# Kernel tuning notes

Hardware: AMD Instinct MI355X
Metric: run time of the kernel (lower is better)

## Reference

```python
import jax, jax.numpy as jnp
import numpy as np

B, N, C, S = 16, 1024, 16, 8
TYPE_DIM, TOK_DIM, D, O = 128, 128, 256, 256
NUM_TYPES, NUM_TOKENS, L = 200, 50000, 2
NEG = -1000000000000.0


def setup_inputs() -> dict:
    key = jax.random.key(0)
    ks = jax.random.split(key, 8)
    node_type = jax.random.randint(ks[0], (B, N), 0, NUM_TYPES)
    node_tokens = jax.random.randint(ks[1], (B, N, S), 0, NUM_TOKENS)
    children_index = jax.random.randint(ks[2], (B, N, C), 0, N)
    # padding_idx=0 -> row 0 of both embedding tables is zero
    type_table = (0.02 * jax.random.normal(ks[3], (NUM_TYPES, TYPE_DIM))).at[0].set(0.0)
    token_table = (0.02 * jax.random.normal(ks[4], (NUM_TOKENS, TOK_DIM))).at[0].set(0.0)
    W_parent = 0.02 * jax.random.normal(ks[5], (TYPE_DIM + TOK_DIM, D))
    b_parent = jnp.zeros((D,), jnp.float32)
    conv_w = 0.02 * jax.random.normal(ks[6], (L, 3, D, O))  # stacked [w_t, w_r, w_l] per layer
    conv_b = jnp.zeros((L, O), jnp.float32)
    attn_a = 0.02 * jax.random.normal(ks[7], (O,))
    return dict(node_type=node_type, node_tokens=node_tokens, children_index=children_index,
                type_table=type_table, token_table=token_table, W_parent=W_parent,
                b_parent=b_parent, conv_w=conv_w, conv_b=conv_b, attn_a=attn_a)


def _gather_children(parent, idx):
    # parent: [B,N,Dim]; idx: [B,N,C] with 0 meaning 'no child' (zero vector)
    lookup = parent.at[:, 0, :].set(0.0)
    return jax.vmap(lambda v, i: v[i])(lookup, idx)  # [B,N,C,Dim]


def _tbcnn_coef(children):
    # Standard TBCNN positional coefficients over [parent, child_1..child_C].
    b, n, c = children.shape
    f = jnp.float32
    cmask = (children > 0).astype(f)                                      # [B,N,C]
    mask = jnp.concatenate([jnp.zeros((b, n, 1), f), cmask], axis=2)      # [B,N,C+1]
    eta_t = jnp.concatenate([jnp.ones((b, n, 1), f), jnp.zeros((b, n, c), f)], axis=2)
    num_sib = jnp.sum(cmask, axis=2, keepdims=True)                       # [B,N,1]
    pos = jnp.arange(-1.0, c, dtype=f)                                    # [-1,0,...,C-1]
    child_idx = pos[None, None, :] * mask
    singles = jnp.concatenate([jnp.zeros((b, n, 1), f), jnp.full((b, n, 1), 0.5, f),
                               jnp.zeros((b, n, c - 1), f)], axis=2)
    denom = jnp.maximum(num_sib - 1.0, 1.0)
    eta_r = jnp.where(num_sib == 1.0, singles, mask * child_idx / denom)
    eta_l = (1.0 - eta_t) * (1.0 - eta_r) * mask
    return jnp.stack([eta_t, eta_r, eta_l], axis=3)                       # [B,N,C+1,3]


def _forward(node_type, node_tokens, children_index, type_table, token_table,
             W_parent, b_parent, conv_w, conv_b, attn_a):
    # --- embeddings + parent projection ---
    type_emb = type_table[node_type]                       # [B,N,TYPE_DIM]
    tok_emb = token_table[node_tokens].sum(axis=2)         # [B,N,TOK_DIM] (sum over subtokens)
    parent = jnp.concatenate([type_emb, tok_emb], axis=-1) @ W_parent + b_parent  # [B,N,D]
    # --- tree convolutions ---
    coef = _tbcnn_coef(children_index)                     # [B,N,C+1,3]
    nodes = parent
    ch = _gather_children(nodes, children_index)           # [B,N,C,D]
    n_layers = conv_w.shape[0]
    for l in range(n_layers):
        tree = jnp.concatenate([nodes[:, :, None, :], ch], axis=2)  # [B,N,C+1,D]
        mixed = jnp.einsum('bnck,bncd->bnkd', coef, tree)           # [B,N,3,D]
        nodes = jnp.tanh(jnp.einsum('bnkd,kdo->bno', mixed, conv_w[l]) + conv_b[l])
        if l < n_layers - 1:
            ch = _gather_children(nodes, children_index)
    # --- attention aggregation ---
    m = (node_type != 0)[..., None]                        # [B,N,1] bool
    score = jnp.einsum('bno,o->bn', nodes, attn_a)[..., None]
    score = jnp.where(m, score, NEG)
    w = jax.nn.sigmoid(score)
    code_vector = jnp.mean(nodes * m * w, axis=1)          # [B,O]
    return code_vector, nodes


def reference(node_type, node_tokens, children_index, type_table, token_table,
              W_parent, b_parent, conv_w, conv_b, attn_a):
    return _forward(node_type, node_tokens, children_index, type_table, token_table,
                    W_parent, b_parent, conv_w, conv_b, attn_a)
```

## Files before the change

kernel.cpp:

```cpp
#include <hip/hip_runtime.h>
#include <math.h>

constexpr int Bsz = 16, Nn = 1024, Cc = 16, Ss = 8;
constexpr int BN = Bsz * Nn;
constexpr int EQ = 16;
constexpr int CQ = 32;

typedef __attribute__((ext_vector_type(8))) short bf16x8;
typedef __attribute__((ext_vector_type(4))) float f32x4;
typedef __attribute__((ext_vector_type(4))) unsigned short u16x4;

__device__ inline unsigned short f2bf_rne(float x) {
    unsigned u = __builtin_bit_cast(unsigned, x);
    unsigned r = (u + 0x7FFFu + ((u >> 16) & 1u)) >> 16;
    return (unsigned short)r;
}
__device__ inline float bf2f(unsigned short h) {
    unsigned u = ((unsigned)h) << 16;
    return __builtin_bit_cast(float, u);
}
__device__ inline float fast_tanh(float x) {
    const float ax = fabsf(x);
    const float t  = __expf(-2.f * ax);
    const float r  = __fdividef(1.f - t, 1.f + t);
    return copysignf(r, x);
}

__global__ __launch_bounds__(256) void pack_wp_kernel(
    const float* __restrict__ Wp, unsigned short* __restrict__ wpq)
{
    const int t = blockIdx.x * 256 + threadIdx.x;
    const int col = t & 255;
    const int gg  = (t >> 8) & 3;
    const int kb  = t >> 10;
    const size_t dst = (size_t)t * 8;
    #pragma unroll
    for (int i = 0; i < 8; ++i)
        wpq[dst + i] = f2bf_rne(Wp[(size_t)(kb * 32 + gg * 8 + i) * 256 + col]);
}

__global__ __launch_bounds__(256, 4) void emb_mfma_kernel(
    const int* __restrict__ node_type, const int* __restrict__ node_tokens,
    const float* __restrict__ type_table, const float* __restrict__ token_table,
    const unsigned short* __restrict__ wpq,
    const float* __restrict__ bp,
    unsigned short* __restrict__ outh,
    const float* __restrict__ conv_w,
    unsigned short* __restrict__ whi)
{
    constexpr int AP = 264;
    __shared__ unsigned short A[EQ][AP];

    const int tid  = threadIdx.x;
    const int lane = tid & 63;
    const int w    = tid >> 6;
    const int g0   = blockIdx.x * EQ;

    {
        const int q    = lane & 31;
        const int half = lane >> 5;
        #pragma unroll
        for (int it = 0; it < 4; ++it) {
            const int r = w * 4 + it;
            const int gnode = g0 + r;
            f32x4 acc = (f32x4){0.f, 0.f, 0.f, 0.f};
            #pragma unroll
            for (int s = 0; s < 4; ++s) {
                const int tok = node_tokens[gnode * Ss + half * 4 + s];
                const f32x4 v = *reinterpret_cast<const f32x4*>(
                    token_table + (size_t)tok * 128 + q * 4);
                acc += v;
            }
            f32x4 tot;
            tot.x = acc.x + __shfl_xor(acc.x, 32);
            tot.y = acc.y + __shfl_xor(acc.y, 32);
            tot.z = acc.z + __shfl_xor(acc.z, 32);
            tot.w = acc.w + __shfl_xor(acc.w, 32);
            if (half == 0) {
                const int tt = node_type[gnode];
                const f32x4 tv = *reinterpret_cast<const f32x4*>(
                    type_table + (size_t)tt * 128 + q * 4);
                u16x4 s0;
                s0.x = f2bf_rne(tv.x); s0.y = f2bf_rne(tv.y);
                s0.z = f2bf_rne(tv.z); s0.w = f2bf_rne(tv.w);
                *reinterpret_cast<u16x4*>(&A[r][q * 4]) = s0;
            } else {
                u16x4 s1;
                s1.x = f2bf_rne(tot.x); s1.y = f2bf_rne(tot.y);
                s1.z = f2bf_rne(tot.z); s1.w = f2bf_rne(tot.w);
                *reinterpret_cast<u16x4*>(&A[r][128 + q * 4]) = s1;
            }
        }
    }
    __syncthreads();

    const int colg = w * 64;
    const int rr   = lane & 15;
    const int g    = lane >> 4;

    const unsigned short* pwh = wpq + ((size_t)(g * 256 + colg + rr)) * 8;

    f32x4 acc[4];
    #pragma unroll
    for (int f = 0; f < 4; ++f) acc[f] = (f32x4){0.f, 0.f, 0.f, 0.f};

    bf16x8 bA[4], bB[4];
    #pragma unroll
    for (int f = 0; f < 4; ++f)
        bA[f] = *reinterpret_cast<const bf16x8*>(pwh + f * 128);

    for (int kb = 0; kb < 8; kb += 2) {
        {
            const int o1 = (kb + 1) * 8192;
            #pragma unroll
            for (int f = 0; f < 4; ++f)
                bB[f] = *reinterpret_cast<const bf16x8*>(pwh + o1 + f * 128);
        }
        {
            const int k0 = kb * 32 + g * 8;
            const bf16x8 ah = *reinterpret_cast<const bf16x8*>(&A[rr][k0]);
            #pragma unroll
            for (int f = 0; f < 4; ++f)
                acc[f] = __builtin_amdgcn_mfma_f32_16x16x32_bf16(ah, bA[f], acc[f], 0, 0, 0);
        }
        if (kb + 2 < 8) {
            const int o2 = (kb + 2) * 8192;
            #pragma unroll
            for (int f = 0; f < 4; ++f)
                bA[f] = *reinterpret_cast<const bf16x8*>(pwh + o2 + f * 128);
        }
        {
            const int k0 = (kb + 1) * 32 + g * 8;
            const bf16x8 ah = *reinterpret_cast<const bf16x8*>(&A[rr][k0]);
            #pragma unroll
            for (int f = 0; f < 4; ++f)
                acc[f] = __builtin_amdgcn_mfma_f32_16x16x32_bf16(ah, bB[f], acc[f], 0, 0, 0);
        }
    }

    #pragma unroll
    for (int f = 0; f < 4; ++f) {
        const int col = colg + f * 16 + rr;
        const float bv = bp[col];
        #pragma unroll
        for (int i = 0; i < 4; ++i) {
            const int row = g * 4 + i;
            outh[(size_t)(g0 + row) * 256 + col] = f2bf_rne(acc[f][i] + bv);
        }
    }

    if (blockIdx.x < 192) {
        const int t = blockIdx.x * 256 + tid;
        const int col = t & 255;
        const int gg  = (t >> 8) & 3;
        const int kb  = (t >> 10) % 24;
        const int l   = t / (24 * 4 * 256);
        const float* W = conv_w + (size_t)l * 768 * 256;
        const size_t dst = (size_t)t * 8;
        #pragma unroll
        for (int i = 0; i < 8; ++i)
            whi[dst + i] = f2bf_rne(W[(size_t)(kb * 32 + gg * 8 + i) * 256 + col]);
    }
}

template<int FUSE>
__global__ __launch_bounds__(512, 4) void conv_mfma_kernel(
    const unsigned short* __restrict__ in_h,
    const int* __restrict__ children_index,
    const unsigned short* __restrict__ whi,
    const float* __restrict__ bias,
    unsigned short* __restrict__ out_h,
    float* __restrict__ out_f,
    const int* __restrict__ node_type,
    const float* __restrict__ attn_a,
    float* __restrict__ partial)
{
    constexpr int AP = 776;
    __shared__ unsigned short Ahi[CQ][AP];
    __shared__ unsigned short idx_s[CQ][Cc];
    __shared__ float etar_s[CQ][Cc];
    __shared__ float etal_s[CQ][Cc];
    __shared__ float sc_lds[8][CQ];
    __shared__ float wm_lds[CQ];

    const int tid = threadIdx.x;

    const int P = blockIdx.x;
    const int xx = P & 7;
    const int rst = P >> 3;
    const int j = rst & 31;
    const int yy = rst >> 5;
    const int batch = xx + 8 * yy;
    const int g0 = batch * Nn + j * CQ;
    const unsigned short* inb = in_h + (size_t)batch * Nn * 256;

    {
        const int r = tid >> 4, c = tid & 15;
        idx_s[r][c] = (unsigned short)children_index[(size_t)(g0 + r) * Cc + c];
    }
    __syncthreads();
    {
        const int r = tid >> 4, c = tid & 15;
        int ns = 0;
        #pragma unroll
        for (int q = 0; q < Cc; ++q) ns += (idx_s[r][q] > 0) ? 1 : 0;
        const bool cm = idx_s[r][c] > 0;
        float er;
        if (ns == 1) {
            er = (c == 0) ? 0.5f : 0.f;
        } else {
            const float denom = (float)((ns - 1 > 1) ? (ns - 1) : 1);
            er = (float)c / denom;
        }
        etar_s[r][c] = cm ? er : 0.f;
        etal_s[r][c] = cm ? (1.f - er) : 0.f;
    }
    __syncthreads();

    {
        const int q = tid & 63;
        const int rgrp = tid >> 6;
        #pragma unroll
        for (int rr4 = 0; rr4 < 4; ++rr4) {
            const int r = rgrp * 4 + rr4;
            const u16x4 m0h = *reinterpret_cast<const u16x4*>(
                in_h + (size_t)(g0 + r) * 256 + q * 4);
            float4 m1 = {0.f, 0.f, 0.f, 0.f};
            float4 m2 = {0.f, 0.f, 0.f, 0.f};
            #pragma unroll
            for (int c = 0; c < Cc; ++c) {
                const int ci = idx_s[r][c];
                const u16x4 vh = *reinterpret_cast<const u16x4*>(
                    inb + (size_t)ci * 256 + q * 4);
                const float vx = bf2f(vh.x), vy = bf2f(vh.y);
                const float vz = bf2f(vh.z), vw = bf2f(vh.w);
                const float er = etar_s[r][c];
                const float el = etal_s[r][c];
                m1.x = fmaf(er, vx, m1.x); m1.y = fmaf(er, vy, m1.y);
                m1.z = fmaf(er, vz, m1.z); m1.w = fmaf(er, vw, m1.w);
                m2.x = fmaf(el, vx, m2.x); m2.y = fmaf(el, vy, m2.y);
                m2.z = fmaf(el, vz, m2.z); m2.w = fmaf(el, vw, m2.w);
            }
            u16x4 s1, s2;
            s1.x = f2bf_rne(m1.x); s1.y = f2bf_rne(m1.y);
            s1.z = f2bf_rne(m1.z); s1.w = f2bf_rne(m1.w);
            s2.x = f2bf_rne(m2.x); s2.y = f2bf_rne(m2.y);
            s2.z = f2bf_rne(m2.z); s2.w = f2bf_rne(m2.w);
            *reinterpret_cast<u16x4*>(&Ahi[r][q * 4])       = m0h;
            *reinterpret_cast<u16x4*>(&Ahi[r][256 + q * 4]) = s1;
            *reinterpret_cast<u16x4*>(&Ahi[r][512 + q * 4]) = s2;
        }
    }
    __syncthreads();

    const int lane = tid & 63;
    const int w    = tid >> 6;
    const int colg = w * 32;
    const int rr   = lane & 15;
    const int g    = lane >> 4;

    const unsigned short* pwh = whi + ((size_t)(g * 256 + colg + rr)) * 8;

    f32x4 acc[2][2];
    #pragma unroll
    for (int t = 0; t < 2; ++t)
        #pragma unroll
        for (int f = 0; f < 2; ++f) acc[t][f] = (f32x4){0.f, 0.f, 0.f, 0.f};

    bf16x8 bA[2], bB[2];
    #pragma unroll
    for (int f = 0; f < 2; ++f)
        bA[f] = *reinterpret_cast<const bf16x8*>(pwh + f * 128);

    __builtin_amdgcn_s_setprio(1);
    for (int kb = 0; kb < 24; kb += 2) {
        {
            const int o1 = (kb + 1) * 8192;
            #pragma unroll
            for (int f = 0; f < 2; ++f)
                bB[f] = *reinterpret_cast<const bf16x8*>(pwh + o1 + f * 128);
        }
        {
            const int k0 = kb * 32 + g * 8;
            const bf16x8 a0 = *reinterpret_cast<const bf16x8*>(&Ahi[rr][k0]);
            const bf16x8 a1 = *reinterpret_cast<const bf16x8*>(&Ahi[16 + rr][k0]);
            #pragma unroll
            for (int f = 0; f < 2; ++f) {
                acc[0][f] = __builtin_amdgcn_mfma_f32_16x16x32_bf16(a0, bA[f], acc[0][f], 0, 0, 0);
                acc[1][f] = __builtin_amdgcn_mfma_f32_16x16x32_bf16(a1, bA[f], acc[1][f], 0, 0, 0);
            }
        }
        if (kb + 2 < 24) {
            const int o2 = (kb + 2) * 8192;
            #pragma unroll
            for (int f = 0; f < 2; ++f)
                bA[f] = *reinterpret_cast<const bf16x8*>(pwh + o2 + f * 128);
        }
        {
            const int k0 = (kb + 1) * 32 + g * 8;
            const bf16x8 a0 = *reinterpret_cast<const bf16x8*>(&Ahi[rr][k0]);
            const bf16x8 a1 = *reinterpret_cast<const bf16x8*>(&Ahi[16 + rr][k0]);
            #pragma unroll
            for (int f = 0; f < 2; ++f) {
                acc[0][f] = __builtin_amdgcn_mfma_f32_16x16x32_bf16(a0, bB[f], acc[0][f], 0, 0, 0);
                acc[1][f] = __builtin_amdgcn_mfma_f32_16x16x32_bf16(a1, bB[f], acc[1][f], 0, 0, 0);
            }
        }
    }
    __builtin_amdgcn_s_setprio(0);

    float nd[2][2][4];
    #pragma unroll
    for (int t = 0; t < 2; ++t)
        #pragma unroll
        for (int f = 0; f < 2; ++f) {
            const int col = colg + f * 16 + rr;
            const float bv = bias[col];
            #pragma unroll
            for (int i = 0; i < 4; ++i) {
                const int row = t * 16 + g * 4 + i;
                const float v = fast_tanh(acc[t][f][i] + bv);
                nd[t][f][i] = v;
                if (FUSE) out_f[(size_t)(g0 + row) * 256 + col] = v;
                else      out_h[(size_t)(g0 + row) * 256 + col] = f2bf_rne(v);
            }
        }

    if (FUSE) {
        float av[2];
        #pragma unroll
        for (int f = 0; f < 2; ++f) av[f] = attn_a[colg + f * 16 + rr];

        float s[2][4];
        #pragma unroll
        for (int t = 0; t < 2; ++t)
            #pragma unroll
            for (int i = 0; i < 4; ++i) {
                float v = 0.f;
                #pragma unroll
                for (int f = 0; f < 2; ++f) v = fmaf(nd[t][f][i], av[f], v);
                s[t][i] = v;
            }
        #pragma unroll
        for (int off = 1; off < 16; off <<= 1)
            #pragma unroll
            for (int t = 0; t < 2; ++t)
                #pragma unroll
                for (int i = 0; i < 4; ++i)
                    s[t][i] += __shfl_xor(s[t][i], off, 64);
        if (rr == 0) {
            #pragma unroll
            for (int t = 0; t < 2; ++t)
                #pragma unroll
                for (int i = 0; i < 4; ++i)
                    sc_lds[w][t * 16 + g * 4 + i] = s[t][i];
        }
        __syncthreads();
        if (tid < CQ) {
            float sc = 0.f;
            #pragma unroll
            for (int ww = 0; ww < 8; ++ww) sc += sc_lds[ww][tid];
            float wmv = 0.f;
            if (node_type[g0 + tid] != 0)
                wmv = __fdividef(1.f, 1.f + __expf(-sc));
            wm_lds[tid] = wmv;
        }
        __syncthreads();

        float qf[2];
        #pragma unroll
        for (int f = 0; f < 2; ++f) {
            float v = 0.f;
            #pragma unroll
            for (int t = 0; t < 2; ++t)
                #pragma unroll
                for (int i = 0; i < 4; ++i)
                    v = fmaf(wm_lds[t * 16 + g * 4 + i], nd[t][f][i], v);
            qf[f] = v;
        }
        #pragma unroll
        for (int f = 0; f < 2; ++f) {
            qf[f] += __shfl_xor(qf[f], 16, 64);
            qf[f] += __shfl_xor(qf[f], 32, 64);
        }
        if (g == 0) {
            const int pidx = batch * 32 + j;
            #pragma unroll
            for (int f = 0; f < 2; ++f)
                partial[(size_t)pidx * 256 + colg + f * 16 + rr] = qf[f];
        }
    }
}

__global__ __launch_bounds__(256) void final_kernel(
    const float* __restrict__ partial, float* __restrict__ code)
{
    const int i = blockIdx.x * 256 + threadIdx.x;
    const int b = i >> 8, o = i & 255;
    float acc = 0.f;
    #pragma unroll
    for (int c = 0; c < 32; ++c) acc += partial[(size_t)(b * 32 + c) * 256 + o];
    code[i] = acc * (1.f / 1024.f);
}

extern "C" void kernel_launch(void* const* d_in, const int* in_sizes, int n_in,
                              void* d_out, int out_size, void* d_ws, size_t ws_size,
                              hipStream_t stream)
{
    const int*   node_type   = (const int*)d_in[0];
    const int*   node_tokens = (const int*)d_in[1];
    const int*   children    = (const int*)d_in[2];
    const float* type_table  = (const float*)d_in[3];
    const float* token_table = (const float*)d_in[4];
    const float* Wp          = (const float*)d_in[5];
    const float* bp          = (const float*)d_in[6];
    const float* conv_w      = (const float*)d_in[7];
    const float* conv_b      = (const float*)d_in[8];
    const float* attn_a      = (const float*)d_in[9];

    float* out    = (float*)d_out;
    float* code   = out;
    float* nodesF = out + 4096;

    unsigned short* nodes0 = (unsigned short*)d_ws;
    unsigned short* nodes1 = nodes0 + (size_t)BN * 256;
    float* partial = (float*)(nodes1 + (size_t)BN * 256);
    unsigned short* whi = (unsigned short*)(partial + 512 * 256);
    unsigned short* wpq = whi + 2 * 196608;

    constexpr int LSTRIDE = 196608;

    pack_wp_kernel<<<32, 256, 0, stream>>>(Wp, wpq);

    emb_mfma_kernel<<<BN / EQ, 256, 0, stream>>>(
        node_type, node_tokens, type_table, token_table, wpq, bp, nodes0,
        conv_w, whi);

    conv_mfma_kernel<0><<<BN / CQ, 512, 0, stream>>>(
        nodes0, children, whi, conv_b, nodes1,
        nullptr, nullptr, nullptr, nullptr);

    conv_mfma_kernel<1><<<BN / CQ, 512, 0, stream>>>(
        nodes1, children, whi + LSTRIDE, conv_b + 256, nullptr,
        nodesF, node_type, attn_a, partial);

    final_kernel<<<16, 256, 0, stream>>>(partial, code);
}
```

Measured before the change: 70.55 us.

## Split child-mixing gather into separate kernel feeding a standalone MFMA GEMM

Each fused conv layer is split into two kernels. The first gathers child rows and computes the eta-weighted right/left mixes into a bf16 scratch buffer, using 16-row blocks and packed half2 coefficients. The second loads the parent rows and the mixes into LDS and runs the MFMA GEMM with the tanh and attention epilogue. The aim is to decouple the latency-bound gather from the GEMM so each gets its own occupancy, at the cost of an extra global round trip and extra launches. The scratch buffer reuses the output nodes region, which the second layer later overwrites.

```diff
diff --git a/kernel.cpp b/kernel.cpp
--- a/kernel.cpp
+++ b/kernel.cpp
@@ -1,10 +1,12 @@
 #include <hip/hip_runtime.h>
+#include <hip/hip_fp16.h>
 #include <math.h>
 
 constexpr int Bsz = 16, Nn = 1024, Cc = 16, Ss = 8;
 constexpr int BN = Bsz * Nn;
 constexpr int EQ = 16;
-constexpr int CQ = 32;
+constexpr int MQ = 16;
+constexpr int GQ = 32;
 
 typedef __attribute__((ext_vector_type(8))) short bf16x8;
 typedef __attribute__((ext_vector_type(4))) float f32x4;
@@ -163,35 +165,23 @@
     }
 }
 
-template<int FUSE>
-__global__ __launch_bounds__(512, 4) void conv_mfma_kernel(
+__global__ __launch_bounds__(256, 8) void mixpre_kernel(
     const unsigned short* __restrict__ in_h,
     const int* __restrict__ children_index,
-    const unsigned short* __restrict__ whi,
-    const float* __restrict__ bias,
-    unsigned short* __restrict__ out_h,
-    float* __restrict__ out_f,
-    const int* __restrict__ node_type,
-    const float* __restrict__ attn_a,
-    float* __restrict__ partial)
-{
-    constexpr int AP = 776;
-    __shared__ unsigned short Ahi[CQ][AP];
-    __shared__ unsigned short idx_s[CQ][Cc];
-    __shared__ float etar_s[CQ][Cc];
-    __shared__ float etal_s[CQ][Cc];
-    __shared__ float sc_lds[8][CQ];
-    __shared__ float wm_lds[CQ];
+    unsigned short* __restrict__ m12)
+{
+    __shared__ unsigned short idx_s[MQ][Cc];
+    __shared__ __half2 eta_s[MQ][Cc];
 
     const int tid = threadIdx.x;
 
     const int P = blockIdx.x;
     const int xx = P & 7;
     const int rst = P >> 3;
-    const int j = rst & 31;
-    const int yy = rst >> 5;
+    const int j = rst & 63;
+    const int yy = rst >> 6;
     const int batch = xx + 8 * yy;
-    const int g0 = batch * Nn + j * CQ;
+    const int g0 = batch * Nn + j * MQ;
     const unsigned short* inb = in_h + (size_t)batch * Nn * 256;
 
     {
@@ -212,49 +202,82 @@
             const float denom = (float)((ns - 1 > 1) ? (ns - 1) : 1);
             er = (float)c / denom;
         }
-        etar_s[r][c] = cm ? er : 0.f;
-        etal_s[r][c] = cm ? (1.f - er) : 0.f;
+        eta_s[r][c] = __halves2half2(__float2half(cm ? er : 0.f),
+                                     __float2half(cm ? (1.f - er) : 0.f));
     }
     __syncthreads();
 
-    {
-        const int q = tid & 63;
-        const int rgrp = tid >> 6;
-        #pragma unroll
-        for (int rr4 = 0; rr4 < 4; ++rr4) {
-            const int r = rgrp * 4 + rr4;
-            const u16x4 m0h = *reinterpret_cast<const u16x4*>(
-                in_h + (size_t)(g0 + r) * 256 + q * 4);
-            float4 m1 = {0.f, 0.f, 0.f, 0.f};
-            float4 m2 = {0.f, 0.f, 0.f, 0.f};
-            #pragma unroll
-            for (int c = 0; c < Cc; ++c) {
-                const int ci = idx_s[r][c];
-                const u16x4 vh = *reinterpret_cast<const u16x4*>(
-                    inb + (size_t)ci * 256 + q * 4);
-                const float vx = bf2f(vh.x), vy = bf2f(vh.y);
-                const float vz = bf2f(vh.z), vw = bf2f(vh.w);
-                const float er = etar_s[r][c];
-                const float el = etal_s[r][c];
-                m1.x = fmaf(er, vx, m1.x); m1.y = fmaf(er, vy, m1.y);
-                m1.z = fmaf(er, vz, m1.z); m1.w = fmaf(er, vw, m1.w);
-                m2.x = fmaf(el, vx, m2.x); m2.y = fmaf(el, vy, m2.y);
-                m2.z = fmaf(el, vz, m2.z); m2.w = fmaf(el, vw, m2.w);
-            }
-            u16x4 s1, s2;
-            s1.x = f2bf_rne(m1.x); s1.y = f2bf_rne(m1.y);
-            s1.z = f2bf_rne(m1.z); s1.w = f2bf_rne(m1.w);
-            s2.x = f2bf_rne(m2.x); s2.y = f2bf_rne(m2.y);
-            s2.z = f2bf_rne(m2.z); s2.w = f2bf_rne(m2.w);
-            *reinterpret_cast<u16x4*>(&Ahi[r][q * 4])       = m0h;
-            *reinterpret_cast<u16x4*>(&Ahi[r][256 + q * 4]) = s1;
-            *reinterpret_cast<u16x4*>(&Ahi[r][512 + q * 4]) = s2;
-        }
-    }
-    __syncthreads();
-
+    const int q = tid & 63;
+    const int w = tid >> 6;
+    #pragma unroll
+    for (int r4 = 0; r4 < 4; ++r4) {
+        const int r = w * 4 + r4;
+        f32x4 m1 = (f32x4){0.f, 0.f, 0.f, 0.f};
+        f32x4 m2 = (f32x4){0.f, 0.f, 0.f, 0.f};
+        #pragma unroll
+        for (int c = 0; c < Cc; ++c) {
+            const int ci = idx_s[r][c];
+            const u16x4 vh = *reinterpret_cast<const u16x4*>(
+                inb + (size_t)ci * 256 + q * 4);
+            f32x4 vf;
+            vf.x = bf2f(vh.x); vf.y = bf2f(vh.y);
+            vf.z = bf2f(vh.z); vf.w = bf2f(vh.w);
+            const __half2 e2 = eta_s[r][c];
+            m1 += __low2float(e2)  * vf;
+            m2 += __high2float(e2) * vf;
+        }
+        u16x4 s1, s2;
+        s1.x = f2bf_rne(m1.x); s1.y = f2bf_rne(m1.y);
+        s1.z = f2bf_rne(m1.z); s1.w = f2bf_rne(m1.w);
+        s2.x = f2bf_rne(m2.x); s2.y = f2bf_rne(m2.y);
+        s2.z = f2bf_rne(m2.z); s2.w = f2bf_rne(m2.w);
+        unsigned short* dst = m12 + (size_t)(g0 + r) * 512;
+        *reinterpret_cast<u16x4*>(dst + q * 4)       = s1;
+        *reinterpret_cast<u16x4*>(dst + 256 + q * 4) = s2;
+    }
+}
+
+template<int FUSE>
+__global__ __launch_bounds__(512, 4) void gemmT_kernel(
+    const unsigned short* __restrict__ in_h,
+    const unsigned short* __restrict__ m12,
+    const unsigned short* __restrict__ whi,
+    const float* __restrict__ bias,
+    unsigned short* __restrict__ out_h,
+    float* __restrict__ out_f,
+    const int* __restrict__ node_type,
+    const float* __restrict__ attn_a,
+    float* __restrict__ partial)
+{
+    constexpr int AP = 776;
+    __shared__ unsigned short Ahi[GQ][AP];
+
+    const int tid = threadIdx.x;
     const int lane = tid & 63;
     const int w    = tid >> 6;
+
+    const int P = blockIdx.x;
+    const int xx = P & 7;
+    const int rst = P >> 3;
+    const int j = rst & 31;
+    const int yy = rst >> 5;
+    const int batch = xx + 8 * yy;
+    const int g0 = batch * Nn + j * GQ;
+
+    #pragma unroll
+    for (int r4 = 0; r4 < 4; ++r4) {
+        const int r = w * 4 + r4;
+        const size_t grow = (size_t)(g0 + r);
+        *reinterpret_cast<u16x4*>(&Ahi[r][lane * 4]) =
+            *reinterpret_cast<const u16x4*>(in_h + grow * 256 + lane * 4);
+        const unsigned short* mrow = m12 + grow * 512;
+        *reinterpret_cast<u16x4*>(&Ahi[r][256 + lane * 4]) =
+            *reinterpret_cast<const u16x4*>(mrow + lane * 4);
+        *reinterpret_cast<u16x4*>(&Ahi[r][512 + lane * 4]) =
+            *reinterpret_cast<const u16x4*>(mrow + 256 + lane * 4);
+    }
+    __syncthreads();
+
     const int colg = w * 32;
     const int rr   = lane & 15;
     const int g    = lane >> 4;
@@ -326,7 +349,10 @@
             }
         }
 
-    if (FUSE) {
+    if constexpr (FUSE) {
+        __shared__ float sc_lds[8][GQ];
+        __shared__ float wm_lds[GQ];
+
         float av[2];
         #pragma unroll
         for (int f = 0; f < 2; ++f) av[f] = attn_a[colg + f * 16 + rr];
@@ -356,7 +382,7 @@
                     sc_lds[w][t * 16 + g * 4 + i] = s[t][i];
         }
         __syncthreads();
-        if (tid < CQ) {
+        if (tid < GQ) {
             float sc = 0.f;
             #pragma unroll
             for (int ww = 0; ww < 8; ++ww) sc += sc_lds[ww][tid];
@@ -421,6 +447,7 @@
     float* out    = (float*)d_out;
     float* code   = out;
     float* nodesF = out + 4096;
+    unsigned short* m12 = (unsigned short*)nodesF;
 
     unsigned short* nodes0 = (unsigned short*)d_ws;
     unsigned short* nodes1 = nodes0 + (size_t)BN * 256;
@@ -436,12 +463,14 @@
         node_type, node_tokens, type_table, token_table, wpq, bp, nodes0,
         conv_w, whi);
 
-    conv_mfma_kernel<0><<<BN / CQ, 512, 0, stream>>>(
-        nodes0, children, whi, conv_b, nodes1,
+    mixpre_kernel<<<BN / MQ, 256, 0, stream>>>(nodes0, children, m12);
+    gemmT_kernel<0><<<BN / GQ, 512, 0, stream>>>(
+        nodes0, m12, whi, conv_b, nodes1,
         nullptr, nullptr, nullptr, nullptr);
 
-    conv_mfma_kernel<1><<<BN / CQ, 512, 0, stream>>>(
-        nodes1, children, whi + LSTRIDE, conv_b + 256, nullptr,
+    mixpre_kernel<<<BN / MQ, 256, 0, stream>>>(nodes1, children, m12);
+    gemmT_kernel<1><<<BN / GQ, 512, 0, stream>>>(
+        nodes1, m12, whi + LSTRIDE, conv_b + 256, nullptr,
         nodesF, node_type, attn_a, partial);
 
     final_kernel<<<16, 256, 0, stream>>>(partial, code);
```

Measured after the change: 83.12 us. 1.18x slower.

## Double conv block to 1024 threads, each wave computing 16 output columns

Applied to the files above, without the earlier changes.

The conv kernels now launch 1024 threads per block instead of 512. Each of the 16 waves owns 16 output columns rather than 32 and gathers child rows for 2 nodes instead of 4. The first B-fragment load is hoisted before the barrier so it overlaps the gather phase. The goal is more waves in flight to hide gather and weight-load latency, at the cost of fewer MFMAs per wave, more per-wave overhead, and a launch bound of 1024x8 that may limit registers.

```diff
diff --git a/kernel.cpp b/kernel.cpp
--- a/kernel.cpp
+++ b/kernel.cpp
@@ -164,7 +164,7 @@
 }
 
 template<int FUSE>
-__global__ __launch_bounds__(512, 4) void conv_mfma_kernel(
+__global__ __launch_bounds__(1024, 8) void conv_mfma_kernel(
     const unsigned short* __restrict__ in_h,
     const int* __restrict__ children_index,
     const unsigned short* __restrict__ whi,
@@ -180,10 +180,12 @@
     __shared__ unsigned short idx_s[CQ][Cc];
     __shared__ float etar_s[CQ][Cc];
     __shared__ float etal_s[CQ][Cc];
-    __shared__ float sc_lds[8][CQ];
+    __shared__ float sc_lds[16][CQ];
     __shared__ float wm_lds[CQ];
 
     const int tid = threadIdx.x;
+    const int lane = tid & 63;
+    const int w    = tid >> 6;
 
     const int P = blockIdx.x;
     const int xx = P & 7;
@@ -194,12 +196,12 @@
     const int g0 = batch * Nn + j * CQ;
     const unsigned short* inb = in_h + (size_t)batch * Nn * 256;
 
-    {
+    if (tid < 512) {
         const int r = tid >> 4, c = tid & 15;
         idx_s[r][c] = (unsigned short)children_index[(size_t)(g0 + r) * Cc + c];
     }
     __syncthreads();
-    {
+    if (tid < 512) {
         const int r = tid >> 4, c = tid & 15;
         int ns = 0;
         #pragma unroll
@@ -217,12 +219,16 @@
     }
     __syncthreads();
 
+    const int colg = w * 16;
+    const int rr   = lane & 15;
+    const int g    = lane >> 4;
+    const unsigned short* pwh = whi + ((size_t)(g * 256 + colg + rr)) * 8;
+
     {
         const int q = tid & 63;
-        const int rgrp = tid >> 6;
-        #pragma unroll
-        for (int rr4 = 0; rr4 < 4; ++rr4) {
-            const int r = rgrp * 4 + rr4;
+        #pragma unroll
+        for (int r2 = 0; r2 < 2; ++r2) {
+            const int r = w * 2 + r2;
             const u16x4 m0h = *reinterpret_cast<const u16x4*>(
                 in_h + (size_t)(g0 + r) * 256 + q * 4);
             float4 m1 = {0.f, 0.f, 0.f, 0.f};
@@ -251,96 +257,60 @@
             *reinterpret_cast<u16x4*>(&Ahi[r][512 + q * 4]) = s2;
         }
     }
+
+    bf16x8 bA = *reinterpret_cast<const bf16x8*>(pwh);
     __syncthreads();
 
-    const int lane = tid & 63;
-    const int w    = tid >> 6;
-    const int colg = w * 32;
-    const int rr   = lane & 15;
-    const int g    = lane >> 4;
-
-    const unsigned short* pwh = whi + ((size_t)(g * 256 + colg + rr)) * 8;
-
-    f32x4 acc[2][2];
-    #pragma unroll
-    for (int t = 0; t < 2; ++t)
-        #pragma unroll
-        for (int f = 0; f < 2; ++f) acc[t][f] = (f32x4){0.f, 0.f, 0.f, 0.f};
-
-    bf16x8 bA[2], bB[2];
-    #pragma unroll
-    for (int f = 0; f < 2; ++f)
-        bA[f] = *reinterpret_cast<const bf16x8*>(pwh + f * 128);
+    f32x4 acc[2];
+    acc[0] = (f32x4){0.f, 0.f, 0.f, 0.f};
+    acc[1] = (f32x4){0.f, 0.f, 0.f, 0.f};
+
+    bf16x8 bB;
 
     __builtin_amdgcn_s_setprio(1);
     for (int kb = 0; kb < 24; kb += 2) {
-        {
-            const int o1 = (kb + 1) * 8192;
-            #pragma unroll
-            for (int f = 0; f < 2; ++f)
-                bB[f] = *reinterpret_cast<const bf16x8*>(pwh + o1 + f * 128);
-        }
+        bB = *reinterpret_cast<const bf16x8*>(pwh + (kb + 1) * 8192);
         {
             const int k0 = kb * 32 + g * 8;
             const bf16x8 a0 = *reinterpret_cast<const bf16x8*>(&Ahi[rr][k0]);
             const bf16x8 a1 = *reinterpret_cast<const bf16x8*>(&Ahi[16 + rr][k0]);
-            #pragma unroll
-            for (int f = 0; f < 2; ++f) {
-                acc[0][f] = __builtin_amdgcn_mfma_f32_16x16x32_bf16(a0, bA[f], acc[0][f], 0, 0, 0);
-                acc[1][f] = __builtin_amdgcn_mfma_f32_16x16x32_bf16(a1, bA[f], acc[1][f], 0, 0, 0);
-            }
-        }
-        if (kb + 2 < 24) {
-            const int o2 = (kb + 2) * 8192;
-            #pragma unroll
-            for (int f = 0; f < 2; ++f)
-                bA[f] = *reinterpret_cast<const bf16x8*>(pwh + o2 + f * 128);
-        }
+            acc[0] = __builtin_amdgcn_mfma_f32_16x16x32_bf16(a0, bA, acc[0], 0, 0, 0);
+            acc[1] = __builtin_amdgcn_mfma_f32_16x16x32_bf16(a1, bA, acc[1], 0, 0, 0);
+        }
+        if (kb + 2 < 24)
+            bA = *reinterpret_cast<const bf16x8*>(pwh + (kb + 2) * 8192);
         {
             const int k0 = (kb + 1) * 32 + g * 8;
             const bf16x8 a0 = *reinterpret_cast<const bf16x8*>(&Ahi[rr][k0]);
             const bf16x8 a1 = *reinterpret_cast<const bf16x8*>(&Ahi[16 + rr][k0]);
-            #pragma unroll
-            for (int f = 0; f < 2; ++f) {
-                acc[0][f] = __builtin_amdgcn_mfma_f32_16x16x32_bf16(a0, bB[f], acc[0][f], 0, 0, 0);
-                acc[1][f] = __builtin_amdgcn_mfma_f32_16x16x32_bf16(a1, bB[f], acc[1][f], 0, 0, 0);
-            }
+            acc[0] = __builtin_amdgcn_mfma_f32_16x16x32_bf16(a0, bB, acc[0], 0, 0, 0);
+            acc[1] = __builtin_amdgcn_mfma_f32_16x16x32_bf16(a1, bB, acc[1], 0, 0, 0);
         }
     }
     __builtin_amdgcn_s_setprio(0);
 
-    float nd[2][2][4];
+    const int col = colg + rr;
+    const float bv = bias[col];
+    float nd[2][4];
     #pragma unroll
     for (int t = 0; t < 2; ++t)
         #pragma unroll
-        for (int f = 0; f < 2; ++f) {
-            const int col = colg + f * 16 + rr;
-            const float bv = bias[col];
-            #pragma unroll
-            for (int i = 0; i < 4; ++i) {
-                const int row = t * 16 + g * 4 + i;
-                const float v = fast_tanh(acc[t][f][i] + bv);
-                nd[t][f][i] = v;
-                if (FUSE) out_f[(size_t)(g0 + row) * 256 + col] = v;
-                else      out_h[(size_t)(g0 + row) * 256 + col] = f2bf_rne(v);
-            }
-        }
-
-    if (FUSE) {
-        float av[2];
-        #pragma unroll
-        for (int f = 0; f < 2; ++f) av[f] = attn_a[colg + f * 16 + rr];
-
+        for (int i = 0; i < 4; ++i) {
+            const int row = t * 16 + g * 4 + i;
+            const float v = fast_tanh(acc[t][i] + bv);
+            nd[t][i] = v;
+            if (FUSE) out_f[(size_t)(g0 + row) * 256 + col] = v;
+            else      out_h[(size_t)(g0 + row) * 256 + col] = f2bf_rne(v);
+        }
+
+    if constexpr (FUSE) {
+        const float av = attn_a[col];
         float s[2][4];
         #pragma unroll
         for (int t = 0; t < 2; ++t)
             #pragma unroll
-            for (int i = 0; i < 4; ++i) {
-                float v = 0.f;
-                #pragma unroll
-                for (int f = 0; f < 2; ++f) v = fmaf(nd[t][f][i], av[f], v);
-                s[t][i] = v;
-            }
+            for (int i = 0; i < 4; ++i)
+                s[t][i] = nd[t][i] * av;
         #pragma unroll
         for (int off = 1; off < 16; off <<= 1)
             #pragma unroll
@@ -359,7 +329,7 @@
         if (tid < CQ) {
             float sc = 0.f;
             #pragma unroll
-            for (int ww = 0; ww < 8; ++ww) sc += sc_lds[ww][tid];
+            for (int ww = 0; ww < 16; ++ww) sc += sc_lds[ww][tid];
             float wmv = 0.f;
             if (node_type[g0 + tid] != 0)
                 wmv = __fdividef(1.f, 1.f + __expf(-sc));
@@ -367,27 +337,17 @@
         }
         __syncthreads();
 
-        float qf[2];
-        #pragma unroll
-        for (int f = 0; f < 2; ++f) {
-            float v = 0.f;
-            #pragma unroll
-            for (int t = 0; t < 2; ++t)
-                #pragma unroll
-                for (int i = 0; i < 4; ++i)
-                    v = fmaf(wm_lds[t * 16 + g * 4 + i], nd[t][f][i], v);
-            qf[f] = v;
-        }
-        #pragma unroll
-        for (int f = 0; f < 2; ++f) {
-            qf[f] += __shfl_xor(qf[f], 16, 64);
-            qf[f] += __shfl_xor(qf[f], 32, 64);
-        }
+        float qf = 0.f;
+        #pragma unroll
+        for (int t = 0; t < 2; ++t)
+            #pragma unroll
+            for (int i = 0; i < 4; ++i)
+                qf = fmaf(wm_lds[t * 16 + g * 4 + i], nd[t][i], qf);
+        qf += __shfl_xor(qf, 16, 64);
+        qf += __shfl_xor(qf, 32, 64);
         if (g == 0) {
             const int pidx = batch * 32 + j;
-            #pragma unroll
-            for (int f = 0; f < 2; ++f)
-                partial[(size_t)pidx * 256 + colg + f * 16 + rr] = qf[f];
+            partial[(size_t)pidx * 256 + col] = qf;
         }
     }
 }
@@ -436,11 +396,11 @@
         node_type, node_tokens, type_table, token_table, wpq, bp, nodes0,
         conv_w, whi);
 
-    conv_mfma_kernel<0><<<BN / CQ, 512, 0, stream>>>(
+    conv_mfma_kernel<0><<<BN / CQ, 1024, 0, stream>>>(
         nodes0, children, whi, conv_b, nodes1,
         nullptr, nullptr, nullptr, nullptr);
 
-    conv_mfma_kernel<1><<<BN / CQ, 512, 0, stream>>>(
+    conv_mfma_kernel<1><<<BN / CQ, 1024, 0, stream>>>(
         nodes1, children, whi + LSTRIDE, conv_b + 256, nullptr,
         nodesF, node_type, attn_a, partial);
 
```

Measured after the change: 75.04 us. +6.4%, slower.
